# Optimization experiments

Hardware: AMD Instinct MI355X
Metric: run time of the kernel (lower is better)

The kernel has to match this reference:

```python
import jax, jax.numpy as jnp
import numpy as np

N_FEAT = 12   # feature_size n -> 2^n-1 = 4095 nonempty subsets
BATCH = 64


def _build_fmat(n):
    # Inclusion-exclusion (Moebius) matrix: column 2k sums f(B) over B >= A_k with
    # even |B \ A_k| (positive part), column 2k+1 over odd |B \ A_k| (negative part).
    masks = np.arange(1, 2 ** n, dtype=np.int64)
    mj, mk = masks[:, None], masks[None, :]
    sub = (mj & mk) == mk            # A_k subset-of A_j
    diff = mj & ~mk
    pc = np.zeros_like(diff)
    for b in range(n):
        pc += (diff >> b) & 1        # popcount(|A_j \ A_k|)
    M = np.zeros((2 ** n - 1, 2 * (2 ** n - 1)), dtype=np.float32)
    M[:, 0::2] = (sub & (pc % 2 == 0)).astype(np.float32)
    M[:, 1::2] = (sub & (pc % 2 == 1)).astype(np.float32)
    return M


def setup_inputs() -> dict:
    key = jax.random.key(0)
    k1, k2, k3 = jax.random.split(key, 3)
    n, B = N_FEAT, BATCH
    xl = jax.random.uniform(k1, (B, n), dtype=jnp.float32)
    xu = xl + (1.0 - xl) * jax.random.uniform(k2, (B, n), dtype=jnp.float32)
    x = jnp.concatenate([xl, xu], axis=1)                          # [B, 2n] lower||upper
    ie_vars = jax.random.uniform(k3, (2 ** n - 2, 1), dtype=jnp.float32) * (0.1 / n)
    singles = jnp.array([2 ** b - 1 for b in range(n)])            # singleton masks -> 1/n
    ie_vars = ie_vars.at[singles, 0].set(1.0 / n)
    fmat = jnp.asarray(_build_fmat(n))                             # [4095, 8190]
    return {"x": x, "ie_vars": ie_vars, "fmat": fmat}


def _subset_products(x, n):
    # feats[:, m-1] = prod_{b in mask m} x[:, b]  (algebraic t-norm over subsets)
    masks = jnp.arange(1, 2 ** n)
    feats = jnp.ones((x.shape[0], 2 ** n - 1), x.dtype)
    for b in range(n):  # n static passes over [B, 2^n-1]
        has_b = ((masks >> b) & 1).astype(bool)
        feats = feats * jnp.where(has_b[None, :], x[:, b:b + 1], jnp.ones((), x.dtype))
    return feats


def _build_FM(ie_vars, n):
    # Monotone fuzzy-measure lattice DP: FM[m] = |v[m]| + max_{b in m} FM[m - 2^b],
    # singletons get just |v|; append mu(full set)=1; clamp to 1.
    v = jnp.abs(ie_vars[:, 0])                    # [2^n - 2]
    nV = 2 ** n - 2
    masks = np.arange(1, 2 ** n - 1)              # static predecessor tables
    preds = np.zeros((nV, n), np.int32)
    valid = np.zeros((nV, n), bool)
    for b in range(n):
        has = ((masks >> b) & 1).astype(bool)
        p = masks - (1 << b) - 1                  # var index of mask with bit b removed
        ok = has & (p >= 0)                       # empty-set predecessor excluded
        preds[:, b] = np.where(ok, p, 0)
        valid[:, b] = ok
    preds_j = jnp.asarray(preds)
    valid_j = jnp.asarray(valid)

    def step(fm, i):
        cand = jnp.where(valid_j[i], fm[preds_j[i]], -jnp.inf)
        mx = jnp.max(cand)
        mx = jnp.where(jnp.isfinite(mx), mx, jnp.zeros((), fm.dtype))
        return fm.at[i].set(v[i] + mx), None

    fm, _ = jax.lax.scan(step, jnp.zeros((nV,), v.dtype), jnp.arange(nV))
    FM = jnp.concatenate([fm, jnp.ones((1,), v.dtype)])
    return jnp.minimum(FM, 1.0)[:, None]          # [2^n - 1, 1]


def reference(x, ie_vars, fmat):
    n = x.shape[1] // 2
    datal, datau = x[:, :n], x[:, n:]
    fl = _subset_products(datal, n)               # [B, 2^n-1]
    fu = _subset_products(datau, n)
    FM = _build_FM(ie_vars, n)                    # [2^n-1, 1]
    fl_mt = fl @ fmat                             # [B, 2*(2^n-1)]
    fu_mt = fu @ fmat
    a = fl_mt[:, 0::2] @ FM                       # [B, 1]
    c = fl_mt[:, 1::2] @ FM
    b_ = fu_mt[:, 0::2] @ FM
    d = fu_mt[:, 1::2] @ FM
    left = jnp.minimum(a - c, b_ - d)
    right = b_ - d
    return left, right
```

## Files before the change

kernel.cpp:

```cpp
#include <hip/hip_runtime.h>


#define NB 12
#define NMASK 4096

__global__ __launch_bounds__(1024) void k_build_w(
    const float* __restrict__ ie_vars, float* __restrict__ W) {
  __shared__ float g[NMASK];
  const int tid = threadIdx.x;

  for (int level = 1; level <= NB; ++level) {
    for (int m = tid; m < NMASK; m += 1024) {
      if (m >= 1 && m <= NMASK - 2 && __popc(m) == level) {
        float best = 0.0f;
#pragma unroll
        for (int b = 0; b < NB; ++b) {
          const int p = m - (1 << b);
          if ((m & (1 << b)) && p >= 1) best = fmaxf(best, g[p]);
        }
        g[m] = fabsf(ie_vars[m - 1]) + best;
      }
    }
    __syncthreads();
  }

  for (int m = tid; m < NMASK; m += 1024) {
    float val;
    if (m == 0)                val = 0.0f;
    else if (m == NMASK - 1)   val = 1.0f;
    else                       val = fminf(g[m], 1.0f);
    g[m] = val;
  }
  __syncthreads();

  for (int b = 0; b < NB; ++b) {
    for (int m = tid; m < NMASK; m += 1024) {
      if (m & (1 << b)) g[m] -= g[m ^ (1 << b)];
    }
    __syncthreads();
  }

  for (int m = tid; m < NMASK; m += 1024) W[m] = g[m];
}

__global__ __launch_bounds__(256) void k_batch(
    const float* __restrict__ x, const float* __restrict__ W,
    float* __restrict__ out) {
  const int b = blockIdx.x;
  const int tid = threadIdx.x;

  __shared__ float xs[24];
  if (tid < 24) xs[tid] = x[b * 24 + tid];
  __syncthreads();

  float lowl[16], lowu[16];
  lowl[0] = 1.0f;
  lowu[0] = 1.0f;
#pragma unroll
  for (int m = 1; m < 16; ++m) {
    const int lb = __ffs(m) - 1;
    lowl[m] = lowl[m & (m - 1)] * xs[lb];
    lowu[m] = lowu[m & (m - 1)] * xs[12 + lb];
  }

  const int hm = tid;
  float hl = 1.0f, hu = 1.0f;
#pragma unroll
  for (int bit = 0; bit < 8; ++bit) {
    if (hm & (1 << bit)) {
      hl *= xs[4 + bit];
      hu *= xs[16 + bit];
    }
  }

  const int base = tid << 4;
  float A = 0.0f, B = 0.0f;
#pragma unroll
  for (int k = 0; k < 16; ++k) {
    const float w = W[base + k];
    A = fmaf(hl * lowl[k], w, A);
    B = fmaf(hu * lowu[k], w, B);
  }

#pragma unroll
  for (int off = 32; off > 0; off >>= 1) {
    A += __shfl_down(A, off);
    B += __shfl_down(B, off);
  }
  __shared__ float rA[4], rB[4];
  const int wave = tid >> 6;
  if ((tid & 63) == 0) {
    rA[wave] = A;
    rB[wave] = B;
  }
  __syncthreads();
  if (tid == 0) {
    const float a = rA[0] + rA[1] + rA[2] + rA[3];
    const float bb = rB[0] + rB[1] + rB[2] + rB[3];
    out[b] = fminf(a, bb);
    out[64 + b] = bb;
  }
}

extern "C" void kernel_launch(void* const* d_in, const int* in_sizes, int n_in,
                              void* d_out, int out_size, void* d_ws,
                              size_t ws_size, hipStream_t stream) {
  const float* x  = (const float*)d_in[0];
  const float* ie = (const float*)d_in[1];
  float* W   = (float*)d_ws;
  float* out = (float*)d_out;

  k_build_w<<<1, 1024, 0, stream>>>(ie, W);
  k_batch<<<64, 256, 0, stream>>>(x, W, out);
}
```

Before: 210.1 us.

## Fuse weight build and batch reduction into one single-block kernel

Merges the Moebius-weight construction kernel and the per-batch reduction kernel into one 1024-thread block. The weights stay in shared memory instead of going through a global workspace, and the second launch is removed. The batch work is reorganised so each wave handles one row at a time, building 64-entry low and high product tables and doing a 64x64 outer-product contraction against the shared weights. The cost is that all 64 rows now run serially on a single CU instead of across 64 blocks, with extra block-wide syncs.

```diff
diff --git a/kernel.cpp b/kernel.cpp
--- a/kernel.cpp
+++ b/kernel.cpp
@@ -3,14 +3,26 @@
 
 #define NB 12
 #define NMASK 4096
+#define NTHREADS 1024
+#define NWAVES 16
+#define XS_ELEMS (64 * 24)
 
-__global__ __launch_bounds__(1024) void k_build_w(
-    const float* __restrict__ ie_vars, float* __restrict__ W) {
+__global__ __launch_bounds__(NTHREADS) void k_fused(
+    const float* __restrict__ x,
+    const float* __restrict__ ie_vars,
+    float* __restrict__ out) {
   __shared__ float g[NMASK];
+  __shared__ float xs[XS_ELEMS];
+  __shared__ float tab[NWAVES][4][64];
+
   const int tid = threadIdx.x;
+  const int lane = tid & 63;
+  const int wave = tid >> 6;
+
+  for (int i = tid; i < XS_ELEMS; i += NTHREADS) xs[i] = x[i];
 
   for (int level = 1; level <= NB; ++level) {
-    for (int m = tid; m < NMASK; m += 1024) {
+    for (int m = tid; m < NMASK; m += NTHREADS) {
       if (m >= 1 && m <= NMASK - 2 && __popc(m) == level) {
         float best = 0.0f;
 #pragma unroll
@@ -24,81 +36,66 @@
     __syncthreads();
   }
 
-  for (int m = tid; m < NMASK; m += 1024) {
+  for (int m = tid; m < NMASK; m += NTHREADS) {
     float val;
-    if (m == 0)                val = 0.0f;
-    else if (m == NMASK - 1)   val = 1.0f;
-    else                       val = fminf(g[m], 1.0f);
+    if (m == 0)              val = 0.0f;
+    else if (m == NMASK - 1) val = 1.0f;
+    else                     val = fminf(g[m], 1.0f);
     g[m] = val;
   }
   __syncthreads();
 
+#pragma unroll 1
   for (int b = 0; b < NB; ++b) {
-    for (int m = tid; m < NMASK; m += 1024) {
+    for (int m = tid; m < NMASK; m += NTHREADS) {
       if (m & (1 << b)) g[m] -= g[m ^ (1 << b)];
     }
     __syncthreads();
   }
 
-  for (int m = tid; m < NMASK; m += 1024) W[m] = g[m];
-}
+#pragma unroll 1
+  for (int iter = 0; iter < 4; ++iter) {
+    const int row = wave + iter * NWAVES;
+    const float* xr = &xs[row * 24];
 
-__global__ __launch_bounds__(256) void k_batch(
-    const float* __restrict__ x, const float* __restrict__ W,
-    float* __restrict__ out) {
-  const int b = blockIdx.x;
-  const int tid = threadIdx.x;
+    float pLL = 1.0f, pHL = 1.0f, pLU = 1.0f, pHU = 1.0f;
+#pragma unroll
+    for (int b = 0; b < 6; ++b) {
+      if (lane & (1 << b)) {
+        pLL *= xr[b];
+        pHL *= xr[6 + b];
+        pLU *= xr[12 + b];
+        pHU *= xr[18 + b];
+      }
+    }
+    tab[wave][0][lane] = pLL;
+    tab[wave][1][lane] = pHL;
+    tab[wave][2][lane] = pLU;
+    tab[wave][3][lane] = pHU;
+    __syncthreads();
 
-  __shared__ float xs[24];
-  if (tid < 24) xs[tid] = x[b * 24 + tid];
-  __syncthreads();
-
-  float lowl[16], lowu[16];
-  lowl[0] = 1.0f;
-  lowu[0] = 1.0f;
+    const float lowL = tab[wave][0][lane];
+    const float lowU = tab[wave][2][lane];
+    float A = 0.0f, B = 0.0f;
 #pragma unroll
-  for (int m = 1; m < 16; ++m) {
-    const int lb = __ffs(m) - 1;
-    lowl[m] = lowl[m & (m - 1)] * xs[lb];
-    lowu[m] = lowu[m & (m - 1)] * xs[12 + lb];
-  }
-
-  const int hm = tid;
-  float hl = 1.0f, hu = 1.0f;
-#pragma unroll
-  for (int bit = 0; bit < 8; ++bit) {
-    if (hm & (1 << bit)) {
-      hl *= xs[4 + bit];
-      hu *= xs[16 + bit];
+    for (int k = 0; k < 64; ++k) {
+      const float w = g[k * 64 + lane];
+      const float hL = tab[wave][1][k];
+      const float hU = tab[wave][3][k];
+      A = fmaf(lowL * hL, w, A);
+      B = fmaf(lowU * hU, w, B);
     }
-  }
-
-  const int base = tid << 4;
-  float A = 0.0f, B = 0.0f;
-#pragma unroll
-  for (int k = 0; k < 16; ++k) {
-    const float w = W[base + k];
-    A = fmaf(hl * lowl[k], w, A);
-    B = fmaf(hu * lowu[k], w, B);
-  }
 
 #pragma unroll
-  for (int off = 32; off > 0; off >>= 1) {
-    A += __shfl_down(A, off);
-    B += __shfl_down(B, off);
-  }
-  __shared__ float rA[4], rB[4];
-  const int wave = tid >> 6;
-  if ((tid & 63) == 0) {
-    rA[wave] = A;
-    rB[wave] = B;
-  }
-  __syncthreads();
-  if (tid == 0) {
-    const float a = rA[0] + rA[1] + rA[2] + rA[3];
-    const float bb = rB[0] + rB[1] + rB[2] + rB[3];
-    out[b] = fminf(a, bb);
-    out[64 + b] = bb;
+    for (int off = 32; off > 0; off >>= 1) {
+      A += __shfl_down(A, off);
+      B += __shfl_down(B, off);
+    }
+    if (lane == 0) {
+      out[row] = fminf(A, B);
+      out[64 + row] = B;
+    }
+    __syncthreads();
   }
 }
 
@@ -107,9 +104,7 @@
                               size_t ws_size, hipStream_t stream) {
   const float* x  = (const float*)d_in[0];
   const float* ie = (const float*)d_in[1];
-  float* W   = (float*)d_ws;
   float* out = (float*)d_out;
 
-  k_build_w<<<1, 1024, 0, stream>>>(ie, W);
-  k_batch<<<64, 256, 0, stream>>>(x, W, out);
+  k_fused<<<1, NTHREADS, 0, stream>>>(x, ie, out);
 }
```

Result: slower. 221.9 us (+5.6%).
